# Kernel optimization log

Hardware: AMD Instinct MI355X
Metric: run time of the kernel (lower is better)

The kernel has to match this reference:

```python
import jax, jax.numpy as jnp
import numpy as np

B, L, D, H = 4, 2048, 1024, 16
HD = D // H  # head_dim = 64


def setup_inputs() -> dict:
    key = jax.random.key(0)
    k1, k2, k3 = jax.random.split(key, 3)
    scale_in = 1.0 / np.sqrt(D)
    return {
        "x": jax.random.normal(k1, (B, L, D), dtype=jnp.float32),
        "Wqkv": jax.random.normal(k2, (D, 3 * D), dtype=jnp.float32) * scale_in,
        "Wout": jax.random.normal(k3, (D, D), dtype=jnp.float32) * scale_in,
        "bout": jnp.zeros((D,), dtype=jnp.float32),
    }


def reference(x, Wqkv, Wout, bout):
    b, l, d = x.shape
    # QKV projection (no bias): [B, L, 3D] -> [B, L, 3, H, HD]
    qkv = (x @ Wqkv).reshape(b, l, 3, H, HD)
    q, k, v = jnp.moveaxis(qkv, 2, 0)  # each [B, L, H, HD]
    # scaled scores [B, H, L, L]
    scores = jnp.einsum("blhd,bmhd->bhlm", q, k) / jnp.sqrt(jnp.float32(HD))
    causal_mask = jnp.triu(jnp.ones((l, l), dtype=bool), k=1)
    scores = jnp.where(causal_mask, -jnp.inf, scores)
    attn = jax.nn.softmax(scores, axis=-1)
    # dropout p=0.0 (eval-mode reference) -> identity
    out = jnp.einsum("bhlm,bmhd->blhd", attn, v).reshape(b, l, d)
    return out @ Wout + bout
```

## Files before the change

### kernel.cpp

```cpp
#include <hip/hip_runtime.h>

typedef unsigned short ushort_t;
using bf16x8 = __attribute__((ext_vector_type(8))) short;
using f32x4  = __attribute__((ext_vector_type(4))) float;
using f32x16 = __attribute__((ext_vector_type(16))) float;
using u32x4  = __attribute__((ext_vector_type(4))) unsigned int;

#define B_  4
#define L_  2048
#define D_  1024
#define H_  16
#define HD_ 64
#define N3_ 3072
#define M1_ (B_ * L_)

static __device__ __forceinline__ unsigned short f2bf(float f) {
    unsigned int u = __float_as_uint(f);
    unsigned int r = (u + 0x7fffu + ((u >> 16) & 1u)) >> 16;
    return (unsigned short)r;
}

static __device__ __forceinline__ unsigned int pkbf(float lo, float hi) {
    unsigned int r;
    asm("v_cvt_pk_bf16_f32 %0, %1, %2" : "=v"(r) : "v"(lo), "v"(hi));
    return r;
}

static __device__ __forceinline__ void plswap(unsigned int& a, unsigned int& b) {
    asm volatile("v_permlane32_swap_b32 %0, %1" : "+v"(a), "+v"(b));
}

static __device__ __forceinline__ void async16(const void* g, const void* l) {
    __builtin_amdgcn_global_load_lds(
        (const __attribute__((address_space(1))) void*)g,
        (__attribute__((address_space(3))) void*)l, 16, 0, 0);
}

__global__ __launch_bounds__(256) void prep_kernel(
    const float* __restrict__ x, const float* __restrict__ Wqkv,
    const float* __restrict__ Wout, ushort4* __restrict__ xb,
    unsigned short* __restrict__ wqkvT, unsigned short* __restrict__ woutT) {
    __shared__ float tile[32][33];
    const int bid = blockIdx.x;
    const int tid = threadIdx.x;
    if (bid < 8192) {
        const int i = bid * 256 + tid;
        float4 v = ((const float4*)x)[i];
        ushort4 o;
        o.x = f2bf(v.x); o.y = f2bf(v.y); o.z = f2bf(v.z); o.w = f2bf(v.w);
        xb[i] = o;
        return;
    }
    const float* src;
    unsigned short* dst;
    int cols, c0, r0;
    if (bid < 8192 + 3072) {
        const int t = bid - 8192;
        src = Wqkv; dst = wqkvT; cols = N3_;
        c0 = (t % 96) * 32; r0 = (t / 96) * 32;
    } else {
        const int t = bid - 8192 - 3072;
        src = Wout; dst = woutT; cols = D_;
        c0 = (t % 32) * 32; r0 = (t / 32) * 32;
    }
    const int tx = tid & 31, ty = tid >> 5;
    #pragma unroll
    for (int j = 0; j < 32; j += 8)
        tile[ty + j][tx] = src[(size_t)(r0 + ty + j) * cols + c0 + tx];
    __syncthreads();
    #pragma unroll
    for (int j = 0; j < 32; j += 8)
        dst[(size_t)(c0 + ty + j) * D_ + r0 + tx] = f2bf(tile[tx][ty + j]);
}

__global__ __launch_bounds__(512, 4) void gemm256_qkv_kernel(
    const unsigned short* __restrict__ A, const unsigned short* __restrict__ BT,
    unsigned short* __restrict__ qb, unsigned short* __restrict__ kb,
    unsigned short* __restrict__ vb) {
    constexpr int K = 1024, BK = 32, NT = K / BK;
    constexpr int NBX = N3_ / 128;
    constexpr int NWG = (M1_ / 256) * NBX;
    __shared__ __align__(16) unsigned short ldsA[3][256 * BK];
    __shared__ __align__(16) unsigned short ldsB[3][128 * BK];

    const int tid = threadIdx.x;
    const int w = tid >> 6, lane = tid & 63;
    const int wr = w >> 2, wc = w & 3;
    const int lg = lane >> 4, ll = lane & 15;

    const int bid = blockIdx.x;
    const int swz = (bid & 7) * (NWG / 8) + (bid >> 3);
    const int m0 = (swz / NBX) * 256, n0 = (swz % NBX) * 128;

    const int srow = tid >> 2;
    const int scol = (((tid & 3) ^ ((tid >> 3) & 3)) * 8);
    const int rxor = ((ll >> 1) & 3) * 8;

    f32x4 acc[8][2] = {};

    #define STAGE(kt_) do {                                                  \
        const int b3_ = (kt_) % 3;                                           \
        const size_t koff_ = (size_t)(kt_) * BK + scol;                      \
        async16(&A[(size_t)(m0 + srow) * K + koff_],       &ldsA[b3_][tid * 8]);        \
        async16(&A[(size_t)(m0 + 128 + srow) * K + koff_], &ldsA[b3_][4096 + tid * 8]); \
        async16(&BT[(size_t)(n0 + srow) * K + koff_],      &ldsB[b3_][tid * 8]);        \
    } while (0)

    STAGE(0);
    STAGE(1);

    #pragma unroll 1
    for (int kt = 0; kt < NT; ++kt) {
        if (kt + 2 < NT) {
            STAGE(kt + 2);
            asm volatile("s_waitcnt vmcnt(6)" ::: "memory");
        } else if (kt + 1 < NT) {
            asm volatile("s_waitcnt vmcnt(3)" ::: "memory");
        } else {
            asm volatile("s_waitcnt vmcnt(0)" ::: "memory");
        }
        __builtin_amdgcn_s_barrier();
        __builtin_amdgcn_sched_barrier(0);

        const unsigned short* Ab = &ldsA[kt % 3][0];
        const unsigned short* Bb = &ldsB[kt % 3][0];
        bf16x8 bfr[2];
        #pragma unroll
        for (int j = 0; j < 2; ++j)
            bfr[j] = *(const bf16x8*)&Bb[(wc * 32 + j * 16 + ll) * BK + (lg * 8 ^ rxor)];
        bf16x8 af[8];
        #pragma unroll
        for (int i = 0; i < 8; ++i)
            af[i] = *(const bf16x8*)&Ab[(wr * 128 + i * 16 + ll) * BK + (lg * 8 ^ rxor)];

        __builtin_amdgcn_s_setprio(1);
        #pragma unroll
        for (int i = 0; i < 8; ++i)
            #pragma unroll
            for (int j = 0; j < 2; ++j)
                acc[i][j] = __builtin_amdgcn_mfma_f32_16x16x32_bf16(
                    af[i], bfr[j], acc[i][j], 0, 0, 0);
        __builtin_amdgcn_s_setprio(0);
        __builtin_amdgcn_s_barrier();
    }
    #undef STAGE

    const float QSCALE = 0.18033688011112042f;
    #pragma unroll
    for (int mi = 0; mi < 8; ++mi) {
        const int mb = m0 + wr * 128 + mi * 16 + lg * 4;
        #pragma unroll
        for (int ni = 0; ni < 2; ++ni) {
            const int n = n0 + wc * 32 + ni * 16 + ll;
            const int s = n >> 10, h = (n >> 6) & 15, hd = n & 63;
            if (s == 2) {
                const int b = mb >> 11, l = mb & 2047;
                const size_t base = (size_t)(b * H_ + h) * (L_ * HD_);
                ushort4 pk;
                pk.x = f2bf(acc[mi][ni][0]);
                pk.y = f2bf(acc[mi][ni][1]);
                pk.z = f2bf(acc[mi][ni][2]);
                pk.w = f2bf(acc[mi][ni][3]);
                *(ushort4*)&vb[base + (l >> 5) * 2048 + ((l >> 4) & 1) * 1024 +
                               ((l >> 3) & 1) * 512 + hd * 8 + (l & 7)] = pk;
            } else {
                #pragma unroll
                for (int r = 0; r < 4; ++r) {
                    const int m = mb + r;
                    const int b = m >> 11, l = m & 2047;
                    const size_t base = (size_t)(b * H_ + h) * (L_ * HD_);
                    const size_t o = base + (l >> 5) * 2048 + (hd >> 4) * 512 +
                                     ((hd >> 3) & 1) * 256 + (l & 31) * 8 + (hd & 7);
                    float v = acc[mi][ni][r];
                    if (s == 0) qb[o] = f2bf(v * QSCALE);
                    else        kb[o] = f2bf(v);
                }
            }
        }
    }
}

__global__ __launch_bounds__(256) void gemm_bt_kernel(
    const unsigned short* __restrict__ A, const unsigned short* __restrict__ BT,
    float* __restrict__ outp, const float* __restrict__ bias) {
    constexpr int K = 1024;
    __shared__ unsigned short As[128 * 32];
    __shared__ unsigned short Bs[128 * 32];
    const int tid = threadIdx.x, w = tid >> 6, lane = tid & 63;
    const int m0 = blockIdx.y * 128, n0 = blockIdx.x * 128;
    const int wm = (w >> 1) * 64, wn = (w & 1) * 64;
    const int lg = lane >> 4, ll = lane & 15;
    const int scol = (((lane & 3) ^ ((lane >> 3) & 3)) * 8);
    const int rxor = ((ll >> 1) & 3) * 8;

    f32x4 acc[4][4] = {};

    for (int k0 = 0; k0 < K; k0 += 32) {
        #pragma unroll
        for (int j = 0; j < 2; ++j) {
            int row = w * 32 + j * 16 + (lane >> 2);
            async16(&A[(size_t)(m0 + row) * K + k0 + scol], &As[(w * 32 + j * 16) * 32]);
            async16(&BT[(size_t)(n0 + row) * K + k0 + scol], &Bs[(w * 32 + j * 16) * 32]);
        }
        __syncthreads();
        bf16x8 af[4], bfr[4];
        #pragma unroll
        for (int i = 0; i < 4; ++i) {
            af[i]  = *(const bf16x8*)&As[(wm + i * 16 + ll) * 32 + (lg * 8 ^ rxor)];
            bfr[i] = *(const bf16x8*)&Bs[(wn + i * 16 + ll) * 32 + (lg * 8 ^ rxor)];
        }
        #pragma unroll
        for (int mi = 0; mi < 4; ++mi)
            #pragma unroll
            for (int ni = 0; ni < 4; ++ni)
                acc[mi][ni] = __builtin_amdgcn_mfma_f32_16x16x32_bf16(
                    af[mi], bfr[ni], acc[mi][ni], 0, 0, 0);
        __syncthreads();
    }

    #pragma unroll
    for (int mi = 0; mi < 4; ++mi)
        #pragma unroll
        for (int ni = 0; ni < 4; ++ni)
            #pragma unroll
            for (int r = 0; r < 4; ++r) {
                int m = m0 + wm + mi * 16 + lg * 4 + r;
                int n = n0 + wn + ni * 16 + ll;
                outp[(size_t)m * D_ + n] = acc[mi][ni][r] + bias[n];
            }
}

__global__ __launch_bounds__(512, 4) void attn_kernel(
    const unsigned short* __restrict__ qbuf, const unsigned short* __restrict__ kbuf,
    const unsigned short* __restrict__ vbuf, unsigned short* __restrict__ obuf) {
    __shared__ float Xo[4][64][33];
    __shared__ float Xs[4][64];
    __shared__ float Sdl[4][32];

    const int tid = threadIdx.x;
    const int w = tid >> 6, lane = tid & 63;
    const int p = w >> 1, s = w & 1;
    const int lq = lane & 31;
    const int hi = lane >> 5;

    const int bid = blockIdx.x;
    const int grp = bid >> 6;
    const int bh  = bid & 63;
    const int qt  = (15 - grp) * 4 + p;
    const int q0  = qt * 32;

    const unsigned short* Qf = qbuf + (size_t)bh * (L_ * HD_);
    const unsigned short* Kf = kbuf + (size_t)bh * (L_ * HD_);
    const unsigned short* Vf = vbuf + (size_t)bh * (L_ * HD_);

    bf16x8 qf[4];
    #pragma unroll
    for (int c = 0; c < 4; ++c)
        qf[c] = *(const bf16x8*)&Qf[qt * 2048 + c * 512 + hi * 256 + lq * 8];

    f32x16 oa0 = {}, oa1 = {};
    float sden = 0.f;

    bf16x8 kf[4];
    if (s <= qt) {
        #pragma unroll
        for (int c = 0; c < 4; ++c)
            kf[c] = *(const bf16x8*)&Kf[s * 2048 + c * 512 + hi * 256 + lq * 8];
    }

    #pragma unroll 1
    for (int t = s; t <= qt; t += 2) {
        bf16x8 v0f[2], v1f[2];
        #pragma unroll
        for (int c = 0; c < 2; ++c) {
            v0f[c] = *(const bf16x8*)&Vf[t * 2048 + c * 1024 + hi * 512 + lq * 8];
            v1f[c] = *(const bf16x8*)&Vf[t * 2048 + c * 1024 + hi * 512 + 256 + lq * 8];
        }
        bf16x8 nk[4];
        const bool more = (t + 2 <= qt);
        if (more) {
            #pragma unroll
            for (int c = 0; c < 4; ++c)
                nk[c] = *(const bf16x8*)&Kf[(t + 2) * 2048 + c * 512 + hi * 256 + lq * 8];
        }

        f32x16 st = {};
        __builtin_amdgcn_s_setprio(1);
        #pragma unroll
        for (int c = 0; c < 4; ++c)
            st = __builtin_amdgcn_mfma_f32_32x32x16_bf16(kf[c], qf[c], st, 0, 0, 0);
        __builtin_amdgcn_s_setprio(0);

        float pp[16];
        float rs = 0.f;
        const bool diag = (t == qt);
        #pragma unroll
        for (int r = 0; r < 16; ++r) {
            float pv = exp2f(st[r]);
            if (diag) {
                int kv = (r & 3) + 8 * (r >> 2) + 4 * hi;
                if (kv > lq) pv = 0.f;
            }
            pp[r] = pv;
            rs += pv;
        }
        rs += __shfl_xor(rs, 32);
        sden += rs;

        unsigned int a0 = pkbf(pp[0],  pp[1]),  a1 = pkbf(pp[2],  pp[3]);
        unsigned int b0 = pkbf(pp[4],  pp[5]),  b1 = pkbf(pp[6],  pp[7]);
        unsigned int c0 = pkbf(pp[8],  pp[9]),  c1 = pkbf(pp[10], pp[11]);
        unsigned int d0 = pkbf(pp[12], pp[13]), d1 = pkbf(pp[14], pp[15]);
        plswap(a0, b0); plswap(a1, b1); plswap(c0, d0); plswap(c1, d1);
        u32x4 t0 = {a0, a1, b0, b1};
        u32x4 t1 = {c0, c1, d0, d1};
        bf16x8 pa0 = __builtin_bit_cast(bf16x8, t0);
        bf16x8 pa1 = __builtin_bit_cast(bf16x8, t1);

        __builtin_amdgcn_s_setprio(1);
        oa0 = __builtin_amdgcn_mfma_f32_32x32x16_bf16(pa0, v0f[0], oa0, 0, 0, 0);
        oa1 = __builtin_amdgcn_mfma_f32_32x32x16_bf16(pa0, v1f[0], oa1, 0, 0, 0);
        oa0 = __builtin_amdgcn_mfma_f32_32x32x16_bf16(pa1, v0f[1], oa0, 0, 0, 0);
        oa1 = __builtin_amdgcn_mfma_f32_32x32x16_bf16(pa1, v1f[1], oa1, 0, 0, 0);
        __builtin_amdgcn_s_setprio(0);

        if (more) {
            #pragma unroll
            for (int c = 0; c < 4; ++c) kf[c] = nk[c];
        }
    }

    if (s == 1) {
        #pragma unroll
        for (int r = 0; r < 16; ++r) {
            Xo[p][lane][r]      = oa0[r];
            Xo[p][lane][16 + r] = oa1[r];
        }
        Xs[p][lane] = sden;
    }
    __syncthreads();
    if (s == 0) {
        #pragma unroll
        for (int r = 0; r < 16; ++r) {
            oa0[r] += Xo[p][lane][r];
            oa1[r] += Xo[p][lane][16 + r];
        }
        sden += Xs[p][lane];

        if (hi == 0) Sdl[p][lq] = 1.0f / sden;
        __builtin_amdgcn_s_waitcnt(0);

        const int b = bh >> 4, h = bh & 15;
        #pragma unroll
        for (int r = 0; r < 16; ++r) {
            int q = (r & 3) + 8 * (r >> 2) + 4 * hi;
            float inv = Sdl[p][q];
            size_t row = (size_t)(b * L_ + q0 + q) * D_ + h * HD_;
            obuf[row + lq]      = f2bf(oa0[r] * inv);
            obuf[row + 32 + lq] = f2bf(oa1[r] * inv);
        }
    }
}

extern "C" void kernel_launch(void* const* d_in, const int* in_sizes, int n_in,
                              void* d_out, int out_size, void* d_ws, size_t ws_size,
                              hipStream_t stream) {
    const float* x    = (const float*)d_in[0];
    const float* Wqkv = (const float*)d_in[1];
    const float* Wout = (const float*)d_in[2];
    const float* bout = (const float*)d_in[3];
    float* out = (float*)d_out;

    char* ws = (char*)d_ws;
    size_t off = 0;
    unsigned short* xb     = (unsigned short*)(ws + off); off += (size_t)M1_ * D_ * 2;
    unsigned short* wqkvT  = (unsigned short*)(ws + off); off += (size_t)N3_ * D_ * 2;
    unsigned short* woutT  = (unsigned short*)(ws + off); off += (size_t)D_ * D_ * 2;
    unsigned short* qb     = (unsigned short*)(ws + off); off += (size_t)B_ * H_ * L_ * HD_ * 2;
    unsigned short* kb     = (unsigned short*)(ws + off); off += (size_t)B_ * H_ * L_ * HD_ * 2;
    unsigned short* vb     = (unsigned short*)(ws + off); off += (size_t)B_ * H_ * L_ * HD_ * 2;
    unsigned short* attnb  = (unsigned short*)(ws + off); off += (size_t)M1_ * D_ * 2;

    prep_kernel<<<dim3(8192 + 3072 + 1024), 256, 0, stream>>>(
        x, Wqkv, Wout, (ushort4*)xb, wqkvT, woutT);

    gemm256_qkv_kernel<<<dim3((M1_ / 256) * (N3_ / 128)), 512, 0, stream>>>(
        xb, wqkvT, qb, kb, vb);

    attn_kernel<<<dim3(16 * 64), 512, 0, stream>>>(qb, kb, vb, attnb);

    gemm_bt_kernel<<<dim3(D_ / 128, M1_ / 128), 256, 0, stream>>>(
        attnb, woutT, out, bout);
}
```

Measured before the change: 175.4 us.

## Split attention KV loop across four waves with balanced causal query-tile pairing

Each block now handles two query tiles (g and 63-g) instead of four consecutive ones, and each query tile is processed by four waves that stride over KV tiles by four rather than two. The grid doubles to 2048 blocks. Pairing short and long causal rows gives each block an even amount of work and more parallelism per tile. The cost is a two-level LDS reduction of the partial outputs with extra __syncthreads.

New measurement: 187.0 us. 6.6% more time.

```diff
diff --git a/kernel.cpp b/kernel.cpp
--- a/kernel.cpp
+++ b/kernel.cpp
@@ -233,21 +233,21 @@
 __global__ __launch_bounds__(512, 4) void attn_kernel(
     const unsigned short* __restrict__ qbuf, const unsigned short* __restrict__ kbuf,
     const unsigned short* __restrict__ vbuf, unsigned short* __restrict__ obuf) {
-    __shared__ float Xo[4][64][33];
-    __shared__ float Xs[4][64];
-    __shared__ float Sdl[4][32];
+    __shared__ float Xo[2][2][64][33];
+    __shared__ float Xs[2][2][64];
+    __shared__ float Sdl[2][32];
 
     const int tid = threadIdx.x;
     const int w = tid >> 6, lane = tid & 63;
-    const int p = w >> 1, s = w & 1;
+    const int qsel = w >> 2, s = w & 3;
     const int lq = lane & 31;
     const int hi = lane >> 5;
 
     const int bid = blockIdx.x;
-    const int grp = bid >> 6;
-    const int bh  = bid & 63;
-    const int qt  = (15 - grp) * 4 + p;
-    const int q0  = qt * 32;
+    const int g  = bid >> 6;
+    const int bh = bid & 63;
+    const int qt = qsel ? (63 - g) : g;
+    const int q0 = qt * 32;
 
     const unsigned short* Qf = qbuf + (size_t)bh * (L_ * HD_);
     const unsigned short* Kf = kbuf + (size_t)bh * (L_ * HD_);
@@ -269,7 +269,7 @@
     }
 
     #pragma unroll 1
-    for (int t = s; t <= qt; t += 2) {
+    for (int t = s; t <= qt; t += 4) {
         bf16x8 v0f[2], v1f[2];
         #pragma unroll
         for (int c = 0; c < 2; ++c) {
@@ -277,11 +277,11 @@
             v1f[c] = *(const bf16x8*)&Vf[t * 2048 + c * 1024 + hi * 512 + 256 + lq * 8];
         }
         bf16x8 nk[4];
-        const bool more = (t + 2 <= qt);
+        const bool more = (t + 4 <= qt);
         if (more) {
             #pragma unroll
             for (int c = 0; c < 4; ++c)
-                nk[c] = *(const bf16x8*)&Kf[(t + 2) * 2048 + c * 512 + hi * 256 + lq * 8];
+                nk[c] = *(const bf16x8*)&Kf[(t + 4) * 2048 + c * 512 + hi * 256 + lq * 8];
         }
 
         f32x16 st = {};
@@ -330,31 +330,51 @@
         }
     }
 
-    if (s == 1) {
-        #pragma unroll
-        for (int r = 0; r < 16; ++r) {
-            Xo[p][lane][r]      = oa0[r];
-            Xo[p][lane][16 + r] = oa1[r];
-        }
-        Xs[p][lane] = sden;
+    if (s == 1 || s == 3) {
+        const int slot = s >> 1;
+        #pragma unroll
+        for (int r = 0; r < 16; ++r) {
+            Xo[qsel][slot][lane][r]      = oa0[r];
+            Xo[qsel][slot][lane][16 + r] = oa1[r];
+        }
+        Xs[qsel][slot][lane] = sden;
+    }
+    __syncthreads();
+    if (s == 0 || s == 2) {
+        const int slot = s >> 1;
+        #pragma unroll
+        for (int r = 0; r < 16; ++r) {
+            oa0[r] += Xo[qsel][slot][lane][r];
+            oa1[r] += Xo[qsel][slot][lane][16 + r];
+        }
+        sden += Xs[qsel][slot][lane];
+    }
+    __syncthreads();
+    if (s == 2) {
+        #pragma unroll
+        for (int r = 0; r < 16; ++r) {
+            Xo[qsel][1][lane][r]      = oa0[r];
+            Xo[qsel][1][lane][16 + r] = oa1[r];
+        }
+        Xs[qsel][1][lane] = sden;
     }
     __syncthreads();
     if (s == 0) {
         #pragma unroll
         for (int r = 0; r < 16; ++r) {
-            oa0[r] += Xo[p][lane][r];
-            oa1[r] += Xo[p][lane][16 + r];
-        }
-        sden += Xs[p][lane];
-
-        if (hi == 0) Sdl[p][lq] = 1.0f / sden;
+            oa0[r] += Xo[qsel][1][lane][r];
+            oa1[r] += Xo[qsel][1][lane][16 + r];
+        }
+        sden += Xs[qsel][1][lane];
+
+        if (hi == 0) Sdl[qsel][lq] = 1.0f / sden;
         __builtin_amdgcn_s_waitcnt(0);
 
         const int b = bh >> 4, h = bh & 15;
         #pragma unroll
         for (int r = 0; r < 16; ++r) {
             int q = (r & 3) + 8 * (r >> 2) + 4 * hi;
-            float inv = Sdl[p][q];
+            float inv = Sdl[qsel][q];
             size_t row = (size_t)(b * L_ + q0 + q) * D_ + h * HD_;
             obuf[row + lq]      = f2bf(oa0[r] * inv);
             obuf[row + 32 + lq] = f2bf(oa1[r] * inv);
@@ -387,7 +407,7 @@
     gemm256_qkv_kernel<<<dim3((M1_ / 256) * (N3_ / 128)), 512, 0, stream>>>(
         xb, wqkvT, qb, kb, vb);
 
-    attn_kernel<<<dim3(16 * 64), 512, 0, stream>>>(qb, kb, vb, attnb);
+    attn_kernel<<<dim3(32 * 64), 512, 0, stream>>>(qb, kb, vb, attnb);
 
     gemm_bt_kernel<<<dim3(D_ / 128, M1_ / 128), 256, 0, stream>>>(
         attnb, woutT, out, bout);
```
